# Kernel tuning notes

Hardware: AMD Instinct MI355X
Metric: run time of the kernel (lower is better)

## Reference

```python
import jax, jax.numpy as jnp
import numpy as np

T, N, F, H, C = 32, 20000, 128, 128, 10
LN_EPS = 1e-5


def setup_inputs() -> dict:
    key = jax.random.key(0)
    ks = jax.random.split(key, 11)
    u = lambda k, shp, bound: jax.random.uniform(k, shp, jnp.float32, -bound, bound)
    bh = 1.0 / np.sqrt(H)  # torch RNNCell / Linear init scale
    return {
        "X": jax.random.normal(ks[0], (T, N, F), jnp.float32),
        "W_ih": u(ks[1], (H, F), bh),
        "W_hh": u(ks[2], (H, H), bh),
        "b_ih": u(ks[3], (H,), bh),
        "b_hh": u(ks[4], (H,), bh),
        "ln_gamma": jnp.ones((H,), jnp.float32),
        "ln_beta": jnp.zeros((H,), jnp.float32),
        "attn_W": u(ks[5], (1, H), bh),
        "attn_b": u(ks[6], (1,), bh),
        "dense_W": u(ks[7], (C, H), bh),
        "dense_b": u(ks[8], (C,), bh),
    }


def reference(X, W_ih, W_hh, b_ih, b_hh, ln_gamma, ln_beta, attn_W, attn_b, dense_W, dense_b):
    # --- R: initial hidden (no ReLU, as in source init branch) ---
    h0 = X[0] @ W_ih.T + b_hh + b_ih  # (N, H)

    def step(h, x):
        h_new = jax.nn.relu(x @ W_ih.T + b_ih + h @ W_hh.T + b_hh)
        return h_new, h_new

    _, outs = jax.lax.scan(step, h0, X)  # (T, N, H)

    # LayerNorm over last dim (dropout is identity in eval / p=0)
    mu = jnp.mean(outs, axis=-1, keepdims=True)
    var = jnp.var(outs, axis=-1, keepdims=True)
    outs = (outs - mu) * jax.lax.rsqrt(var + LN_EPS) * ln_gamma + ln_beta

    # --- attn: linear -> softmax over time axis 0 ---
    a = jax.nn.softmax(outs @ attn_W.T + attn_b, axis=0)  # (T, N, 1)

    # --- dense: linear -> weight by attention -> sum over time ---
    d = outs @ dense_W.T + dense_b  # (T, N, C)
    return jnp.sum(d * a, axis=0)  # (N, C)
```

## Files before the change

### kernel.cpp

```cpp
#include <hip/hip_runtime.h>
#include <math.h>

#define TT 32
#define NN 20000
#define FF 128
#define HH 128
#define CC 10
#define RPB 32
#define NTHREADS 512

typedef __attribute__((ext_vector_type(8))) _Float16 f16x8;
typedef __attribute__((ext_vector_type(4))) _Float16 f16x4;
typedef __attribute__((ext_vector_type(4))) float f32x4;

#define PLANE_LO 16384
#define Y_OFF    32768
#define WS_LO    32768
#define WS_D     65536
#define A_ADDR(row, chunk) (((row) << 9) + ((((chunk) ^ ((row) & 15))) << 4))
#define Y_ADDR(row, chunk) (Y_OFF + ((row) << 8) + ((((chunk) ^ ((row) & 15))) << 4))

__device__ __forceinline__ void split8(float4 a, float4 b, f16x8* hi, f16x8* lo) {
    float v[8] = {a.x, a.y, a.z, a.w, b.x, b.y, b.z, b.w};
    f16x8 h, l;
#pragma unroll
    for (int j = 0; j < 8; ++j) {
        _Float16 hh = (_Float16)v[j];
        h[j] = hh;
        l[j] = (_Float16)(v[j] - (float)hh);
    }
    *hi = h; *lo = l;
}

__global__ __launch_bounds__(256, 1)
void grn_prep(const float* __restrict__ W_ih,
              const float* __restrict__ W_hh,
              const float* __restrict__ dense_W,
              const float* __restrict__ attn_w,
              _Float16* __restrict__ wsg)
{
    const int i  = blockIdx.x * 256 + threadIdx.x;
    const int kg = i & 31;
    const int c  = i >> 5;
    const int k0 = kg << 3;
    const float* src = (k0 < 128) ? (W_ih + c * 128 + k0)
                                  : (W_hh + c * 128 + (k0 - 128));
    float4 w0 = *(const float4*)src;
    float4 w1 = *(const float4*)(src + 4);
    f16x8 whi, wlo;
    split8(w0, w1, &whi, &wlo);
    *(f16x8*)(wsg + kg * 1024 + c * 8)         = whi;
    *(f16x8*)(wsg + WS_LO + kg * 1024 + c * 8) = wlo;

    if (i < 256) {
        const int kg2 = i >> 4;
        const int cc  = i & 15;
        f16x8 d;
#pragma unroll
        for (int j = 0; j < 8; ++j) {
            const int k = (kg2 << 3) + j;
            float v = 0.f;
            if (cc < 10)       v = dense_W[cc * 128 + k];
            else if (cc == 10) v = attn_w[k];
            d[j] = (_Float16)v;
        }
        *(f16x8*)(wsg + WS_D + kg2 * 128 + cc * 8) = d;
    }
}

__global__ __launch_bounds__(NTHREADS, 1)
void grn_r11(const float* __restrict__ X,
             const _Float16* __restrict__ wsg,
             const float* __restrict__ b_ih,
             const float* __restrict__ b_hh,
             const float* __restrict__ gamma,
             const float* __restrict__ beta,
             const float* __restrict__ dense_b,
             float* __restrict__ out)
{
    __shared__ __align__(16) char smem[40960];
    char* smA = smem;

    const int tid  = threadIdx.x;
    const int lane = tid & 63;
    const int wave = tid >> 6;
    const int n0   = blockIdx.x * RPB;

    f16x8 Whi[8], Wlo[8];
    {
        const int c = (wave << 4) + (lane & 15);
#pragma unroll
        for (int ks = 0; ks < 8; ++ks) {
            const int kc = (ks << 2) + (lane >> 4);
            Whi[ks] = *(const f16x8*)(wsg + kc * 1024 + c * 8);
            Wlo[ks] = *(const f16x8*)(wsg + WS_LO + kc * 1024 + c * 8);
        }
    }

    f16x8 wd[4];
    {
        const int cc = lane & 15;
#pragma unroll
        for (int ks = 0; ks < 4; ++ks) {
            const int kc = (ks << 2) + (lane >> 4);
            wd[ks] = *(const f16x8*)(wsg + WS_D + kc * 128 + cc * 8);
        }
    }

    const int c0 = (wave << 4) + ((lane >> 4) << 2);
    f32x4 bias4;
    {
        float4 bi = *(const float4*)(b_ih + c0);
        float4 bh = *(const float4*)(b_hh + c0);
        bias4[0] = bi.x + bh.x; bias4[1] = bi.y + bh.y;
        bias4[2] = bi.z + bh.z; bias4[3] = bi.w + bh.w;
    }
    const int kch   = 16 + (c0 >> 3);
    const int c0off = (c0 & 4) << 1;

    const int lrow = tid >> 4;
    const int lc   = tid & 15;
    float g[8], bb[8];
    {
        const int cb = lc << 3;
        float4 g0 = *(const float4*)(gamma + cb);
        float4 g1 = *(const float4*)(gamma + cb + 4);
        float4 b0 = *(const float4*)(beta  + cb);
        float4 b1 = *(const float4*)(beta  + cb + 4);
        g[0]=g0.x; g[1]=g0.y; g[2]=g0.z; g[3]=g0.w;
        g[4]=g1.x; g[5]=g1.y; g[6]=g1.z; g[7]=g1.w;
        bb[0]=b0.x; bb[1]=b0.y; bb[2]=b0.z; bb[3]=b0.w;
        bb[4]=b1.x; bb[5]=b1.y; bb[6]=b1.z; bb[7]=b1.w;
    }

    {
        const float* xs0 = X + (size_t)(n0 + lrow) * FF + (lc << 3);
        float4 p0 = *(const float4*)xs0;
        float4 p1 = *(const float4*)(xs0 + 4);
        f16x8 hi, lo;
        split8(p0, p1, &hi, &lo);
        *(f16x8*)(smA + A_ADDR(lrow, lc)) = hi;
        *(f16x8*)(smA + PLANE_LO + A_ADDR(lrow, lc)) = lo;
        f16x8 z;
#pragma unroll
        for (int j = 0; j < 8; ++j) z[j] = (_Float16)0.f;
        for (int i = tid; i < 1024; i += NTHREADS) {
            const int pl  = i >> 9;
            const int row = (i >> 4) & 31;
            const int ch  = 16 + (i & 15);
            *(f16x8*)(smA + pl * PLANE_LO + (row << 9) + (ch << 4)) = z;
        }
    }
    __syncthreads();

    {
        f32x4 acc[2];
        acc[0] = (f32x4){0.f,0.f,0.f,0.f};
        acc[1] = (f32x4){0.f,0.f,0.f,0.f};
#pragma unroll
        for (int ks = 0; ks < 8; ++ks) {
            const int kc = (ks << 2) + (lane >> 4);
            f16x8 a0h = *(const f16x8*)(smA + A_ADDR(lane & 15, kc));
            f16x8 a0l = *(const f16x8*)(smA + PLANE_LO + A_ADDR(lane & 15, kc));
            f16x8 a1h = *(const f16x8*)(smA + A_ADDR(16 + (lane & 15), kc));
            f16x8 a1l = *(const f16x8*)(smA + PLANE_LO + A_ADDR(16 + (lane & 15), kc));
            acc[0] = __builtin_amdgcn_mfma_f32_16x16x32_f16(Whi[ks], a0h, acc[0], 0, 0, 0);
            acc[0] = __builtin_amdgcn_mfma_f32_16x16x32_f16(Whi[ks], a0l, acc[0], 0, 0, 0);
            acc[0] = __builtin_amdgcn_mfma_f32_16x16x32_f16(Wlo[ks], a0h, acc[0], 0, 0, 0);
            acc[1] = __builtin_amdgcn_mfma_f32_16x16x32_f16(Whi[ks], a1h, acc[1], 0, 0, 0);
            acc[1] = __builtin_amdgcn_mfma_f32_16x16x32_f16(Whi[ks], a1l, acc[1], 0, 0, 0);
            acc[1] = __builtin_amdgcn_mfma_f32_16x16x32_f16(Wlo[ks], a1h, acc[1], 0, 0, 0);
        }
        __syncthreads();
#pragma unroll
        for (int mt = 0; mt < 2; ++mt) {
            const int row = (lane & 15) + (mt << 4);
            f16x4 hi4, lo4;
#pragma unroll
            for (int q = 0; q < 4; ++q) {
                const float v = acc[mt][q] + bias4[q];
                _Float16 hh = (_Float16)v;
                hi4[q] = hh;
                lo4[q] = (_Float16)(v - (float)hh);
            }
            const int addr = (row << 9) + (((kch ^ (row & 15))) << 4) + c0off;
            *(f16x4*)(smA + addr) = hi4;
            *(f16x4*)(smA + PLANE_LO + addr) = lo4;
        }
    }
    __syncthreads();

    float stm[4], stz[4], sta[4];
#pragma unroll
    for (int s = 0; s < 4; ++s) { stm[s] = -INFINITY; stz[s] = 0.f; sta[s] = 0.f; }

    for (int t = 0; t < TT; ++t) {
        float4 p0, p1;
        if (t < TT - 1) {
            const float* xs0 = X + ((size_t)(t + 1) * NN + n0 + lrow) * FF + (lc << 3);
            p0 = *(const float4*)xs0;
            p1 = *(const float4*)(xs0 + 4);
        }

        f32x4 acc[2];
        acc[0] = (f32x4){0.f,0.f,0.f,0.f};
        acc[1] = (f32x4){0.f,0.f,0.f,0.f};
#pragma unroll
        for (int ks = 0; ks < 8; ++ks) {
            const int kc = (ks << 2) + (lane >> 4);
            f16x8 a0h = *(const f16x8*)(smA + A_ADDR(lane & 15, kc));
            f16x8 a0l = *(const f16x8*)(smA + PLANE_LO + A_ADDR(lane & 15, kc));
            f16x8 a1h = *(const f16x8*)(smA + A_ADDR(16 + (lane & 15), kc));
            f16x8 a1l = *(const f16x8*)(smA + PLANE_LO + A_ADDR(16 + (lane & 15), kc));
            acc[0] = __builtin_amdgcn_mfma_f32_16x16x32_f16(Whi[ks], a0h, acc[0], 0, 0, 0);
            acc[0] = __builtin_amdgcn_mfma_f32_16x16x32_f16(Whi[ks], a0l, acc[0], 0, 0, 0);
            acc[0] = __builtin_amdgcn_mfma_f32_16x16x32_f16(Wlo[ks], a0h, acc[0], 0, 0, 0);
            acc[1] = __builtin_amdgcn_mfma_f32_16x16x32_f16(Whi[ks], a1h, acc[1], 0, 0, 0);
            acc[1] = __builtin_amdgcn_mfma_f32_16x16x32_f16(Whi[ks], a1l, acc[1], 0, 0, 0);
            acc[1] = __builtin_amdgcn_mfma_f32_16x16x32_f16(Wlo[ks], a1h, acc[1], 0, 0, 0);
        }
        __syncthreads();

#pragma unroll
        for (int mt = 0; mt < 2; ++mt) {
            const int row = (lane & 15) + (mt << 4);
            f16x4 hi4, lo4;
#pragma unroll
            for (int q = 0; q < 4; ++q) {
                const float v = fmaxf(acc[mt][q] + bias4[q], 0.f);
                _Float16 hh = (_Float16)v;
                hi4[q] = hh;
                lo4[q] = (_Float16)(v - (float)hh);
            }
            const int addr = (row << 9) + (((kch ^ (row & 15))) << 4) + c0off;
            *(f16x4*)(smA + addr) = hi4;
            *(f16x4*)(smA + PLANE_LO + addr) = lo4;
        }
        if (t < TT - 1) {
            f16x8 hi, lo;
            split8(p0, p1, &hi, &lo);
            *(f16x8*)(smA + A_ADDR(lrow, lc)) = hi;
            *(f16x8*)(smA + PLANE_LO + A_ADDR(lrow, lc)) = lo;
        }
        __syncthreads();

        {
            f16x8 hv = *(const f16x8*)(smA + A_ADDR(lrow, 16 + lc));
            float v[8];
            float s1 = 0.f, s2 = 0.f;
#pragma unroll
            for (int j = 0; j < 8; ++j) { v[j] = (float)hv[j]; }
#pragma unroll
            for (int j = 0; j < 8; ++j) { s1 += v[j]; s2 += v[j] * v[j]; }
            s1 += __shfl_xor(s1, 1); s2 += __shfl_xor(s2, 1);
            s1 += __shfl_xor(s1, 2); s2 += __shfl_xor(s2, 2);
            s1 += __shfl_xor(s1, 4); s2 += __shfl_xor(s2, 4);
            s1 += __shfl_xor(s1, 8); s2 += __shfl_xor(s2, 8);
            const float mu  = s1 * (1.f / 128.f);
            const float var = s2 * (1.f / 128.f) - mu * mu;
            const float rsi = rsqrtf(var + 1e-5f);
            f16x8 y;
#pragma unroll
            for (int j = 0; j < 8; ++j)
                y[j] = (_Float16)((v[j] - mu) * rsi * g[j] + bb[j]);
            *(f16x8*)(smem + Y_ADDR(lrow, lc)) = y;
        }
        __syncthreads();

        if (wave < 2) {
            f32x4 acc2 = (f32x4){0.f,0.f,0.f,0.f};
#pragma unroll
            for (int ks = 0; ks < 4; ++ks) {
                const int kc = (ks << 2) + (lane >> 4);
                f16x8 a = *(const f16x8*)(smem + Y_ADDR((wave << 4) + (lane & 15), kc));
                acc2 = __builtin_amdgcn_mfma_f32_16x16x32_f16(a, wd[ks], acc2, 0, 0, 0);
            }
#pragma unroll
            for (int r = 0; r < 4; ++r) {
                const float dval = acc2[r];
                const float lg = __shfl(dval, (lane & 48) + 10);
                const float mn = fmaxf(stm[r], lg);
                const float sc = __expf(stm[r] - mn);
                const float e  = __expf(lg - mn);
                stz[r] = stz[r] * sc + e;
                sta[r] = sta[r] * sc + e * dval;
                stm[r] = mn;
            }
        }
    }

    if (wave < 2) {
        const int c = lane & 15;
        if (c < CC) {
            const float db = dense_b[c];
#pragma unroll
            for (int r = 0; r < 4; ++r) {
                const int row = (wave << 4) + ((lane >> 4) << 2) + r;
                out[(size_t)(n0 + row) * CC + c] = sta[r] / stz[r] + db;
            }
        }
    }
}

extern "C" void kernel_launch(void* const* d_in, const int* in_sizes, int n_in,
                              void* d_out, int out_size, void* d_ws, size_t ws_size,
                              hipStream_t stream) {
    const float* X      = (const float*)d_in[0];
    const float* W_ih   = (const float*)d_in[1];
    const float* W_hh   = (const float*)d_in[2];
    const float* b_ih   = (const float*)d_in[3];
    const float* b_hh   = (const float*)d_in[4];
    const float* gamma  = (const float*)d_in[5];
    const float* beta   = (const float*)d_in[6];
    const float* attn_w = (const float*)d_in[7];
    const float* dW     = (const float*)d_in[9];
    const float* db     = (const float*)d_in[10];
    float* out = (float*)d_out;
    _Float16* wsg = (_Float16*)d_ws;
    (void)in_sizes; (void)n_in; (void)out_size; (void)ws_size;

    grn_prep<<<dim3(16), dim3(256), 0, stream>>>(W_ih, W_hh, dW, attn_w, wsg);
    grn_r11<<<dim3(NN / RPB), dim3(NTHREADS), 0, stream>>>(
        X, wsg, b_ih, b_hh, gamma, beta, db, out);
}
```

Before: 211.2 us.

## Switch recurrence to 32x32x16 MFMA with 4 waves and split accumulators

Switches the per-step recurrent GEMM from 16x16x32 MFMA tiles on 8 waves to 32x32x16 MFMA tiles on 4 waves (256 threads). Each wave now covers a 32x32 output tile and holds twice as many weight fragments in registers. The hi and lo products go into separate accumulators, which shortens the chain of dependent MFMAs. LayerNorm and X staging are reworked so each thread handles 16 elements or two rows. The block keeps the same rows with half the threads, so latency hiding drops and register pressure rises.

Measured after the change: 293.2 us. 1.39x slower.

```diff
diff --git a/kernel.cpp b/kernel.cpp
--- a/kernel.cpp
+++ b/kernel.cpp
@@ -7,11 +7,12 @@
 #define HH 128
 #define CC 10
 #define RPB 32
-#define NTHREADS 512
+#define NTHREADS 256
 
 typedef __attribute__((ext_vector_type(8))) _Float16 f16x8;
 typedef __attribute__((ext_vector_type(4))) _Float16 f16x4;
-typedef __attribute__((ext_vector_type(4))) float f32x4;
+typedef __attribute__((ext_vector_type(4))) float  f32x4;
+typedef __attribute__((ext_vector_type(16))) float f32x16;
 
 #define PLANE_LO 16384
 #define Y_OFF    32768
@@ -69,7 +70,7 @@
 }
 
 __global__ __launch_bounds__(NTHREADS, 1)
-void grn_r11(const float* __restrict__ X,
+void grn_r12(const float* __restrict__ X,
              const _Float16* __restrict__ wsg,
              const float* __restrict__ b_ih,
              const float* __restrict__ b_hh,
@@ -86,14 +87,14 @@
     const int wave = tid >> 6;
     const int n0   = blockIdx.x * RPB;
 
-    f16x8 Whi[8], Wlo[8];
-    {
-        const int c = (wave << 4) + (lane & 15);
-#pragma unroll
-        for (int ks = 0; ks < 8; ++ks) {
-            const int kc = (ks << 2) + (lane >> 4);
-            Whi[ks] = *(const f16x8*)(wsg + kc * 1024 + c * 8);
-            Wlo[ks] = *(const f16x8*)(wsg + WS_LO + kc * 1024 + c * 8);
+    f16x8 Whi[16], Wlo[16];
+    {
+        const int cW = (wave << 5) + (lane & 31);
+#pragma unroll
+        for (int kstep = 0; kstep < 16; ++kstep) {
+            const int kc = (kstep << 1) + (lane >> 5);
+            Whi[kstep] = *(const f16x8*)(wsg + kc * 1024 + cW * 8);
+            Wlo[kstep] = *(const f16x8*)(wsg + WS_LO + kc * 1024 + cW * 8);
         }
     }
 
@@ -107,40 +108,45 @@
         }
     }
 
-    const int c0 = (wave << 4) + ((lane >> 4) << 2);
-    f32x4 bias4;
-    {
-        float4 bi = *(const float4*)(b_ih + c0);
-        float4 bh = *(const float4*)(b_hh + c0);
-        bias4[0] = bi.x + bh.x; bias4[1] = bi.y + bh.y;
-        bias4[2] = bi.z + bh.z; bias4[3] = bi.w + bh.w;
-    }
-    const int kch   = 16 + (c0 >> 3);
-    const int c0off = (c0 & 4) << 1;
-
-    const int lrow = tid >> 4;
-    const int lc   = tid & 15;
-    float g[8], bb[8];
-    {
-        const int cb = lc << 3;
-        float4 g0 = *(const float4*)(gamma + cb);
-        float4 g1 = *(const float4*)(gamma + cb + 4);
-        float4 b0 = *(const float4*)(beta  + cb);
-        float4 b1 = *(const float4*)(beta  + cb + 4);
-        g[0]=g0.x; g[1]=g0.y; g[2]=g0.z; g[3]=g0.w;
-        g[4]=g1.x; g[5]=g1.y; g[6]=g1.z; g[7]=g1.w;
-        bb[0]=b0.x; bb[1]=b0.y; bb[2]=b0.z; bb[3]=b0.w;
-        bb[4]=b1.x; bb[5]=b1.y; bb[6]=b1.z; bb[7]=b1.w;
-    }
-
-    {
-        const float* xs0 = X + (size_t)(n0 + lrow) * FF + (lc << 3);
+    float4 bias4g[4];
+#pragma unroll
+    for (int gq = 0; gq < 4; ++gq) {
+        const int cb = (wave << 5) + (gq << 3) + ((lane >> 5) << 2);
+        float4 bi = *(const float4*)(b_ih + cb);
+        float4 bh = *(const float4*)(b_hh + cb);
+        bias4g[gq] = make_float4(bi.x + bh.x, bi.y + bh.y, bi.z + bh.z, bi.w + bh.w);
+    }
+
+    const int lrow = tid >> 3;
+    const int l8   = tid & 7;
+    float g[16], bb[16];
+    {
+        const int cb = l8 << 4;
+#pragma unroll
+        for (int q = 0; q < 4; ++q) {
+            float4 gv = *(const float4*)(gamma + cb + q * 4);
+            float4 bv = *(const float4*)(beta  + cb + q * 4);
+            g[q*4+0]=gv.x; g[q*4+1]=gv.y; g[q*4+2]=gv.z; g[q*4+3]=gv.w;
+            bb[q*4+0]=bv.x; bb[q*4+1]=bv.y; bb[q*4+2]=bv.z; bb[q*4+3]=bv.w;
+        }
+    }
+
+    const int xrow = tid >> 4;
+    const int xch  = tid & 15;
+
+    {
+        const float* xs0 = X + (size_t)(n0 + xrow) * FF + (xch << 3);
         float4 p0 = *(const float4*)xs0;
         float4 p1 = *(const float4*)(xs0 + 4);
+        float4 p2 = *(const float4*)(xs0 + 16 * FF);
+        float4 p3 = *(const float4*)(xs0 + 16 * FF + 4);
         f16x8 hi, lo;
         split8(p0, p1, &hi, &lo);
-        *(f16x8*)(smA + A_ADDR(lrow, lc)) = hi;
-        *(f16x8*)(smA + PLANE_LO + A_ADDR(lrow, lc)) = lo;
+        *(f16x8*)(smA + A_ADDR(xrow, xch)) = hi;
+        *(f16x8*)(smA + PLANE_LO + A_ADDR(xrow, xch)) = lo;
+        split8(p2, p3, &hi, &lo);
+        *(f16x8*)(smA + A_ADDR(xrow + 16, xch)) = hi;
+        *(f16x8*)(smA + PLANE_LO + A_ADDR(xrow + 16, xch)) = lo;
         f16x8 z;
 #pragma unroll
         for (int j = 0; j < 8; ++j) z[j] = (_Float16)0.f;
@@ -153,37 +159,36 @@
     }
     __syncthreads();
 
-    {
-        f32x4 acc[2];
-        acc[0] = (f32x4){0.f,0.f,0.f,0.f};
-        acc[1] = (f32x4){0.f,0.f,0.f,0.f};
-#pragma unroll
-        for (int ks = 0; ks < 8; ++ks) {
-            const int kc = (ks << 2) + (lane >> 4);
-            f16x8 a0h = *(const f16x8*)(smA + A_ADDR(lane & 15, kc));
-            f16x8 a0l = *(const f16x8*)(smA + PLANE_LO + A_ADDR(lane & 15, kc));
-            f16x8 a1h = *(const f16x8*)(smA + A_ADDR(16 + (lane & 15), kc));
-            f16x8 a1l = *(const f16x8*)(smA + PLANE_LO + A_ADDR(16 + (lane & 15), kc));
-            acc[0] = __builtin_amdgcn_mfma_f32_16x16x32_f16(Whi[ks], a0h, acc[0], 0, 0, 0);
-            acc[0] = __builtin_amdgcn_mfma_f32_16x16x32_f16(Whi[ks], a0l, acc[0], 0, 0, 0);
-            acc[0] = __builtin_amdgcn_mfma_f32_16x16x32_f16(Wlo[ks], a0h, acc[0], 0, 0, 0);
-            acc[1] = __builtin_amdgcn_mfma_f32_16x16x32_f16(Whi[ks], a1h, acc[1], 0, 0, 0);
-            acc[1] = __builtin_amdgcn_mfma_f32_16x16x32_f16(Whi[ks], a1l, acc[1], 0, 0, 0);
-            acc[1] = __builtin_amdgcn_mfma_f32_16x16x32_f16(Wlo[ks], a1h, acc[1], 0, 0, 0);
+    const int rowA = lane & 31;
+
+    {
+        f32x16 acch, accl;
+#pragma unroll
+        for (int r = 0; r < 16; ++r) { acch[r] = 0.f; accl[r] = 0.f; }
+#pragma unroll
+        for (int kstep = 0; kstep < 16; ++kstep) {
+            const int ch = (kstep << 1) + (lane >> 5);
+            f16x8 ah = *(const f16x8*)(smA + A_ADDR(rowA, ch));
+            f16x8 al = *(const f16x8*)(smA + PLANE_LO + A_ADDR(rowA, ch));
+            acch = __builtin_amdgcn_mfma_f32_32x32x16_f16(Whi[kstep], ah, acch, 0, 0, 0);
+            accl = __builtin_amdgcn_mfma_f32_32x32x16_f16(Whi[kstep], al, accl, 0, 0, 0);
+            accl = __builtin_amdgcn_mfma_f32_32x32x16_f16(Wlo[kstep], ah, accl, 0, 0, 0);
         }
         __syncthreads();
 #pragma unroll
-        for (int mt = 0; mt < 2; ++mt) {
-            const int row = (lane & 15) + (mt << 4);
+        for (int gq = 0; gq < 4; ++gq) {
+            const int colb = (wave << 5) + (gq << 3) + ((lane >> 5) << 2);
             f16x4 hi4, lo4;
 #pragma unroll
             for (int q = 0; q < 4; ++q) {
-                const float v = acc[mt][q] + bias4[q];
+                const float v = acch[gq*4+q] + accl[gq*4+q]
+                              + ((const float*)&bias4g[gq])[q];
                 _Float16 hh = (_Float16)v;
                 hi4[q] = hh;
                 lo4[q] = (_Float16)(v - (float)hh);
             }
-            const int addr = (row << 9) + (((kch ^ (row & 15))) << 4) + c0off;
+            const int kchw = 16 + (colb >> 3);
+            const int addr = (rowA << 9) + ((kchw ^ (rowA & 15)) << 4) + ((colb & 7) << 1);
             *(f16x4*)(smA + addr) = hi4;
             *(f16x4*)(smA + PLANE_LO + addr) = lo4;
         }
@@ -195,75 +200,81 @@
     for (int s = 0; s < 4; ++s) { stm[s] = -INFINITY; stz[s] = 0.f; sta[s] = 0.f; }
 
     for (int t = 0; t < TT; ++t) {
-        float4 p0, p1;
+        float4 p0, p1, p2, p3;
         if (t < TT - 1) {
-            const float* xs0 = X + ((size_t)(t + 1) * NN + n0 + lrow) * FF + (lc << 3);
+            const float* xs0 = X + ((size_t)(t + 1) * NN + n0 + xrow) * FF + (xch << 3);
             p0 = *(const float4*)xs0;
             p1 = *(const float4*)(xs0 + 4);
-        }
-
-        f32x4 acc[2];
-        acc[0] = (f32x4){0.f,0.f,0.f,0.f};
-        acc[1] = (f32x4){0.f,0.f,0.f,0.f};
-#pragma unroll
-        for (int ks = 0; ks < 8; ++ks) {
-            const int kc = (ks << 2) + (lane >> 4);
-            f16x8 a0h = *(const f16x8*)(smA + A_ADDR(lane & 15, kc));
-            f16x8 a0l = *(const f16x8*)(smA + PLANE_LO + A_ADDR(lane & 15, kc));
-            f16x8 a1h = *(const f16x8*)(smA + A_ADDR(16 + (lane & 15), kc));
-            f16x8 a1l = *(const f16x8*)(smA + PLANE_LO + A_ADDR(16 + (lane & 15), kc));
-            acc[0] = __builtin_amdgcn_mfma_f32_16x16x32_f16(Whi[ks], a0h, acc[0], 0, 0, 0);
-            acc[0] = __builtin_amdgcn_mfma_f32_16x16x32_f16(Whi[ks], a0l, acc[0], 0, 0, 0);
-            acc[0] = __builtin_amdgcn_mfma_f32_16x16x32_f16(Wlo[ks], a0h, acc[0], 0, 0, 0);
-            acc[1] = __builtin_amdgcn_mfma_f32_16x16x32_f16(Whi[ks], a1h, acc[1], 0, 0, 0);
-            acc[1] = __builtin_amdgcn_mfma_f32_16x16x32_f16(Whi[ks], a1l, acc[1], 0, 0, 0);
-            acc[1] = __builtin_amdgcn_mfma_f32_16x16x32_f16(Wlo[ks], a1h, acc[1], 0, 0, 0);
+            p2 = *(const float4*)(xs0 + 16 * FF);
+            p3 = *(const float4*)(xs0 + 16 * FF + 4);
+        }
+
+        f32x16 acch, accl;
+#pragma unroll
+        for (int r = 0; r < 16; ++r) { acch[r] = 0.f; accl[r] = 0.f; }
+#pragma unroll
+        for (int kstep = 0; kstep < 16; ++kstep) {
+            const int ch = (kstep << 1) + (lane >> 5);
+            f16x8 ah = *(const f16x8*)(smA + A_ADDR(rowA, ch));
+            f16x8 al = *(const f16x8*)(smA + PLANE_LO + A_ADDR(rowA, ch));
+            acch = __builtin_amdgcn_mfma_f32_32x32x16_f16(Whi[kstep], ah, acch, 0, 0, 0);
+            accl = __builtin_amdgcn_mfma_f32_32x32x16_f16(Whi[kstep], al, accl, 0, 0, 0);
+            accl = __builtin_amdgcn_mfma_f32_32x32x16_f16(Wlo[kstep], ah, accl, 0, 0, 0);
         }
         __syncthreads();
 
 #pragma unroll
-        for (int mt = 0; mt < 2; ++mt) {
-            const int row = (lane & 15) + (mt << 4);
+        for (int gq = 0; gq < 4; ++gq) {
+            const int colb = (wave << 5) + (gq << 3) + ((lane >> 5) << 2);
             f16x4 hi4, lo4;
 #pragma unroll
             for (int q = 0; q < 4; ++q) {
-                const float v = fmaxf(acc[mt][q] + bias4[q], 0.f);
+                const float v = fmaxf(acch[gq*4+q] + accl[gq*4+q]
+                                      + ((const float*)&bias4g[gq])[q], 0.f);
                 _Float16 hh = (_Float16)v;
                 hi4[q] = hh;
                 lo4[q] = (_Float16)(v - (float)hh);
             }
-            const int addr = (row << 9) + (((kch ^ (row & 15))) << 4) + c0off;
+            const int kchw = 16 + (colb >> 3);
+            const int addr = (rowA << 9) + ((kchw ^ (rowA & 15)) << 4) + ((colb & 7) << 1);
             *(f16x4*)(smA + addr) = hi4;
             *(f16x4*)(smA + PLANE_LO + addr) = lo4;
         }
         if (t < TT - 1) {
             f16x8 hi, lo;
             split8(p0, p1, &hi, &lo);
-            *(f16x8*)(smA + A_ADDR(lrow, lc)) = hi;
-            *(f16x8*)(smA + PLANE_LO + A_ADDR(lrow, lc)) = lo;
+            *(f16x8*)(smA + A_ADDR(xrow, xch)) = hi;
+            *(f16x8*)(smA + PLANE_LO + A_ADDR(xrow, xch)) = lo;
+            split8(p2, p3, &hi, &lo);
+            *(f16x8*)(smA + A_ADDR(xrow + 16, xch)) = hi;
+            *(f16x8*)(smA + PLANE_LO + A_ADDR(xrow + 16, xch)) = lo;
         }
         __syncthreads();
 
         {
-            f16x8 hv = *(const f16x8*)(smA + A_ADDR(lrow, 16 + lc));
-            float v[8];
+            f16x8 h0v = *(const f16x8*)(smA + A_ADDR(lrow, 16 + (l8 << 1)));
+            f16x8 h1v = *(const f16x8*)(smA + A_ADDR(lrow, 16 + (l8 << 1) + 1));
+            float v[16];
             float s1 = 0.f, s2 = 0.f;
 #pragma unroll
-            for (int j = 0; j < 8; ++j) { v[j] = (float)hv[j]; }
-#pragma unroll
-            for (int j = 0; j < 8; ++j) { s1 += v[j]; s2 += v[j] * v[j]; }
+            for (int j = 0; j < 8; ++j) { v[j] = (float)h0v[j]; v[8 + j] = (float)h1v[j]; }
+#pragma unroll
+            for (int j = 0; j < 16; ++j) { s1 += v[j]; s2 += v[j] * v[j]; }
             s1 += __shfl_xor(s1, 1); s2 += __shfl_xor(s2, 1);
             s1 += __shfl_xor(s1, 2); s2 += __shfl_xor(s2, 2);
             s1 += __shfl_xor(s1, 4); s2 += __shfl_xor(s2, 4);
-            s1 += __shfl_xor(s1, 8); s2 += __shfl_xor(s2, 8);
             const float mu  = s1 * (1.f / 128.f);
             const float var = s2 * (1.f / 128.f) - mu * mu;
             const float rsi = rsqrtf(var + 1e-5f);
-            f16x8 y;
+            f16x8 y0, y1;
 #pragma unroll
             for (int j = 0; j < 8; ++j)
-                y[j] = (_Float16)((v[j] - mu) * rsi * g[j] + bb[j]);
-            *(f16x8*)(smem + Y_ADDR(lrow, lc)) = y;
+                y0[j] = (_Float16)((v[j] - mu) * rsi * g[j] + bb[j]);
+#pragma unroll
+            for (int j = 0; j < 8; ++j)
+                y1[j] = (_Float16)((v[8 + j] - mu) * rsi * g[8 + j] + bb[8 + j]);
+            *(f16x8*)(smem + Y_ADDR(lrow, (l8 << 1)))     = y0;
+            *(f16x8*)(smem + Y_ADDR(lrow, (l8 << 1) + 1)) = y1;
         }
         __syncthreads();
 
@@ -320,6 +331,6 @@
     (void)in_sizes; (void)n_in; (void)out_size; (void)ws_size;
 
     grn_prep<<<dim3(16), dim3(256), 0, stream>>>(W_ih, W_hh, dW, attn_w, wsg);
-    grn_r11<<<dim3(NN / RPB), dim3(NTHREADS), 0, stream>>>(
+    grn_r12<<<dim3(NN / RPB), dim3(NTHREADS), 0, stream>>>(
         X, wsg, b_ih, b_hh, gamma, beta, db, out);
 }
```
